# Performance work log

Measured on AMD Instinct MI355X. Metric: run time of the kernel, lower is better.

## Reference

```python
import jax, jax.numpy as jnp
import numpy as np

H_LAT = 64   # latent height (original_shape H)
W_LAT = 64   # latent width  (original_shape W)
COND_LEN = 77  # text tokens per regional condition


def _resize_nearest_exact(m, H, W):
    # matches torch F.interpolate(mode='nearest-exact') for a 2D mask
    h0, w0 = m.shape
    ih = jnp.floor((jnp.arange(H) + 0.5) * (h0 / H)).astype(jnp.int32)
    iw = jnp.floor((jnp.arange(W) + 0.5) * (w0 / W)).astype(jnp.int32)
    return m[ih][:, iw]


def setup_inputs() -> dict:
    key = jax.random.key(0)
    kq, kk, kv, km = jax.random.split(key, 4)
    b, qlen, inner = 2, H_LAT * W_LAT, 512
    klen = 4 * COND_LEN  # 4 regions x 77 tokens
    q = jax.random.normal(kq, (b, qlen, inner), dtype=jnp.float32)
    k = jax.random.normal(kk, (b, klen, inner), dtype=jnp.float32)
    v = jax.random.normal(kv, (b, klen, inner), dtype=jnp.float32)
    dd_masks = jax.random.uniform(km, (4, 32, 32), dtype=jnp.float32)
    # ensure full spatial coverage (region 0 = global) so no softmax row is all-masked
    dd_masks = dd_masks.at[0].set(1.0)
    return {"q": q, "k": k, "v": v, "dd_masks": dd_masks, "heads": 8}


def reference(q, k, v, dd_masks, heads):
    b, qlen, inner = q.shape
    dh = inner // heads
    # [b, heads, seq, dh]
    qh = q.reshape(b, qlen, heads, dh).transpose(0, 2, 1, 3)
    kh = k.reshape(b, -1, heads, dh).transpose(0, 2, 1, 3)
    vh = v.reshape(b, -1, heads, dh).transpose(0, 2, 1, 3)

    # build DenseDiffusion mask: each region mask resized to HxW, flattened,
    # and repeated over that region's COND_LEN key columns
    R = dd_masks.shape[0]
    resized = jax.vmap(lambda m: _resize_nearest_exact(m, H_LAT, W_LAT))(dd_masks)  # [R,H,W]
    flat = resized.reshape(R, H_LAT * W_LAT).T            # [HW, R]
    masks = jnp.repeat(flat, COND_LEN, axis=1)            # [HW, R*COND_LEN]
    mask_bool = masks > 0.5                               # [HW, klen]
    mask_scale = (H_LAT * W_LAT) / jnp.sum(masks, axis=0, keepdims=True)  # [1, klen]

    scale = 1.0 / np.sqrt(dh).astype(np.float32)
    attn = jnp.einsum('bhqd,bhkd->bhqk', qh, kh) * scale  # [b,h,HW,klen]
    attn = attn * mask_scale                              # broadcast over b,h,q
    attn = jnp.where(mask_bool, attn, -jnp.inf)
    w = jax.nn.softmax(attn, axis=-1)
    out = jnp.einsum('bhqk,bhkd->bhqd', w, vh)
    return out.transpose(0, 2, 1, 3).reshape(b, qlen, heads * dh)
```

## Files before the change

kernel.cpp:

```cpp
#include <hip/hip_runtime.h>
#include <hip/hip_bf16.h>

typedef __attribute__((ext_vector_type(8))) short short8;
typedef __attribute__((ext_vector_type(16))) float floatx16;

#define HW_TOK 4096
#define KLEN 308
#define DH 64
#define INNER 512

#define KROWS 320
#define VSTRU 328
#define VBASE (KROWS * 64)
#define KV_TOTAL (VBASE + DH * VSTRU)
#define NW 8

__device__ __forceinline__ unsigned short f2bf(float f) {
    union { float f; unsigned u; } x; x.f = f;
    unsigned u = x.u;
    return (unsigned short)((u + 0x7FFFu + ((u >> 16) & 1u)) >> 16);
}
__device__ __forceinline__ unsigned pk2bf(float a, float b) {
    return ((unsigned)f2bf(b) << 16) | (unsigned)f2bf(a);
}

__global__ __launch_bounds__(512, 1)
void dd_attn_kernel(const float* __restrict__ q,
                    const float* __restrict__ k,
                    const float* __restrict__ v,
                    const float* __restrict__ dd,
                    float* __restrict__ out) {
    __shared__ unsigned short KV[KV_TOTAL];
    __shared__ unsigned short Pb[NW][2][32][32];

    const int tid  = threadIdx.x;
    const int lane = tid & 63;
    const int wave = tid >> 6;
    const int half = lane >> 5;
    const int l31  = lane & 31;
    const int quad = lane >> 4;
    const int l15  = lane & 15;
    const int prot = 8 * ((l31 >> 1) & 7);

    const int bid = blockIdx.x;
    const int bh  = bid >> 4;
    const int grp = bid & 15;
    const int b = bh >> 3, h = bh & 7;

    const float* qp = q + (size_t)b * HW_TOK * INNER + h * DH;
    const float* kp = k + (size_t)b * KLEN * INNER + h * DH;
    const float* vp = v + (size_t)b * KLEN * INNER + h * DH;
    float* op = out + (size_t)b * HW_TOK * INNER + h * DH;

    for (int e = tid; e < KLEN * 32; e += 512) {
        int row = e >> 5, d2 = e & 31;
        float2 f = *(const float2*)(kp + (size_t)row * INNER + 2 * d2);
        int c = d2 >> 2;
        int off = row * 64 + (((c ^ (row & 7)) << 3) | ((d2 & 3) << 1));
        *(unsigned*)&KV[off] = pk2bf(f.x, f.y);
    }
    for (int e = tid; e < 12 * 64; e += 512) KV[KLEN * 64 + e] = 0;

    #pragma unroll
    for (int i = 0; i < 5; ++i) {
        int cq = wave + NW * i;
        float f[8];
        #pragma unroll
        for (int j = 0; j < 8; ++j) {
            int col = cq * 8 + j;
            f[j] = (col < KLEN) ? vp[(size_t)col * INNER + lane] : 0.f;
        }
        union { short8 s; unsigned u[4]; } vv;
        #pragma unroll
        for (int j = 0; j < 4; ++j) vv.u[j] = pk2bf(f[2 * j], f[2 * j + 1]);
        int swz = (cq & ~7) | ((cq ^ (lane & 7)) & 7);
        *(short8*)&KV[VBASE + lane * VSTRU + (swz << 3)] = vv.s;
    }
    float rsum = 0.f;
    {
        const float* dp = dd + quad * 1024 + l15 * 4;
        #pragma unroll
        for (int j = 0; j < 16; ++j) {
            float4 f = *(const float4*)(dp + j * 64);
            rsum += f.x + f.y + f.z + f.w;
        }
        #pragma unroll
        for (int off = 1; off < 16; off <<= 1) rsum += __shfl_xor(rsum, off);
    }
    float rsc[4];
    #pragma unroll
    for (int r = 0; r < 4; ++r)
        rsc[r] = 4096.0f / (4.0f * __shfl(rsum, r * 16 + l15));

    __syncthreads();

    const int q0 = (grp * NW + wave) * 32;
    const int qrow = q0 + l31;

    short8 qb[4];
    const float* qr = qp + (size_t)qrow * INNER;
    #pragma unroll
    for (int ks = 0; ks < 4; ++ks) {
        const float* p0 = qr + ks * 16 + half * 8;
        float4 a = *(const float4*)p0;
        float4 c = *(const float4*)(p0 + 4);
        union { short8 s; unsigned u[4]; } u;
        u.u[0] = pk2bf(a.x, a.y); u.u[1] = pk2bf(a.z, a.w);
        u.u[2] = pk2bf(c.x, c.y); u.u[3] = pk2bf(c.z, c.w);
        qb[ks] = u.s;
    }

    const int mi = (qrow >> 7) * 32 + ((qrow & 63) >> 1);
    float coef[4];
    #pragma unroll
    for (int r = 0; r < 4; ++r)
        coef[r] = (dd[r * 1024 + mi] > 0.5f) ? 0.125f * 1.44269504089f * rsc[r] : -1.0f;

    float l_run = 0.f;
    floatx16 oA[2], oB[2];
    #pragma unroll
    for (int j = 0; j < 16; ++j) { oA[0][j]=0.f; oA[1][j]=0.f; oB[0][j]=0.f; oB[1][j]=0.f; }

    #pragma unroll
    for (int t = 0; t < 10; ++t) {
        const int row = t * 32 + l31;
        floatx16 c;
        #pragma unroll
        for (int j = 0; j < 16; ++j) c[j] = 0.f;
        #pragma unroll
        for (int ks = 0; ks < 4; ++ks) {
            int cc = ks * 2 + half;
            short8 ka = *(const short8*)&KV[row * 64 + ((cc ^ (row & 7)) << 3)];
            c = __builtin_amdgcn_mfma_f32_32x32x16_bf16(ka, qb[ks], c, 0, 0, 0);
        }
        #pragma unroll
        for (int reg = 0; reg < 16; ++reg) {
            const int C0 = t * 32 + (reg & 3) + 8 * (reg >> 2);
            const int C1 = C0 + 4;
            float cfA = (C0 < 77) ? coef[0] : (C0 < 154) ? coef[1]
                      : (C0 < 231) ? coef[2] : (C0 < 308) ? coef[3] : -1.0f;
            float cfB = (C1 < 77) ? coef[0] : (C1 < 154) ? coef[1]
                      : (C1 < 231) ? coef[2] : (C1 < 308) ? coef[3] : -1.0f;
            float cf = half ? cfB : cfA;
            float p = __builtin_amdgcn_exp2f(c[reg] * cf);
            p = (cf > 0.f) ? p : 0.f;
            c[reg] = p;
            l_run += p;
        }
        const int tb = t & 1;
        unsigned short* pr = &Pb[wave][tb][l31][0];
        #pragma unroll
        for (int g = 0; g < 4; ++g) {
            unsigned u0 = pk2bf(c[4 * g],     c[4 * g + 1]);
            unsigned u1 = pk2bf(c[4 * g + 2], c[4 * g + 3]);
            *(uint2*)&pr[(8 * g + 4 * half + prot) & 31] = make_uint2(u0, u1);
        }
        #pragma unroll
        for (int ks2 = 0; ks2 < 2; ++ks2) {
            short8 pb = *(const short8*)&pr[(16 * ks2 + 8 * half + prot) & 31];
            int cc2 = (t * 2 + ks2) * 2 + half;
            #pragma unroll
            for (int mt = 0; mt < 2; ++mt) {
                int vrow = 32 * mt + l31;
                int swz = (cc2 & ~7) | ((cc2 ^ (vrow & 7)) & 7);
                short8 va = *(const short8*)&KV[VBASE + vrow * VSTRU + (swz << 3)];
                if (ks2 == 0)
                    oA[mt] = __builtin_amdgcn_mfma_f32_32x32x16_bf16(va, pb, oA[mt], 0, 0, 0);
                else
                    oB[mt] = __builtin_amdgcn_mfma_f32_32x32x16_bf16(va, pb, oB[mt], 0, 0, 0);
            }
        }
    }

    l_run += __shfl_xor(l_run, 32);
    const float inv = 1.0f / l_run;
    float* o = op + (size_t)qrow * INNER;
    #pragma unroll
    for (int mt = 0; mt < 2; ++mt) {
        #pragma unroll
        for (int g = 0; g < 4; ++g) {
            float4 ov;
            ov.x = (oA[mt][4 * g]     + oB[mt][4 * g])     * inv;
            ov.y = (oA[mt][4 * g + 1] + oB[mt][4 * g + 1]) * inv;
            ov.z = (oA[mt][4 * g + 2] + oB[mt][4 * g + 2]) * inv;
            ov.w = (oA[mt][4 * g + 3] + oB[mt][4 * g + 3]) * inv;
            *(float4*)&o[32 * mt + 8 * g + 4 * half] = ov;
        }
    }
}

extern "C" void kernel_launch(void* const* d_in, const int* in_sizes, int n_in,
                              void* d_out, int out_size, void* d_ws, size_t ws_size,
                              hipStream_t stream) {
    const float* q  = (const float*)d_in[0];
    const float* k  = (const float*)d_in[1];
    const float* v  = (const float*)d_in[2];
    const float* dd = (const float*)d_in[3];
    float* out = (float*)d_out;
    dd_attn_kernel<<<dim3(256), dim3(512), 0, stream>>>(q, k, v, dd, out);
}
```

Before: 103.9 us.

## Pass softmax probabilities via cross-lane shuffles instead of an LDS round trip

Drops the per-wave LDS buffer that held the bf16 probability tile. The P operand for the PV matmul is now built in registers with a 32-lane xor shuffle, and the MFMA operand order is swapped so the output accumulates transposed. That removes LDS writes and reads and one sync point per tile, and frees enough LDS for launch_bounds(512,2). The cost is more shuffle instructions, a tighter VGPR cap that may cause spills, and scalar coalesced output stores with a per-row shuffled normaliser. It also drops the K padding rows; their scores are masked to zero by the select.

Result: faster. 91.06 us (-12.3%).

```diff
diff --git a/kernel.cpp b/kernel.cpp
--- a/kernel.cpp
+++ b/kernel.cpp
@@ -9,9 +9,8 @@
 #define DH 64
 #define INNER 512
 
-#define KROWS 320
 #define VSTRU 328
-#define VBASE (KROWS * 64)
+#define VBASE (KLEN * 64)
 #define KV_TOTAL (VBASE + DH * VSTRU)
 #define NW 8
 
@@ -24,14 +23,13 @@
     return ((unsigned)f2bf(b) << 16) | (unsigned)f2bf(a);
 }
 
-__global__ __launch_bounds__(512, 1)
+__global__ __launch_bounds__(512, 2)
 void dd_attn_kernel(const float* __restrict__ q,
                     const float* __restrict__ k,
                     const float* __restrict__ v,
                     const float* __restrict__ dd,
                     float* __restrict__ out) {
     __shared__ unsigned short KV[KV_TOTAL];
-    __shared__ unsigned short Pb[NW][2][32][32];
 
     const int tid  = threadIdx.x;
     const int lane = tid & 63;
@@ -40,7 +38,6 @@
     const int l31  = lane & 31;
     const int quad = lane >> 4;
     const int l15  = lane & 15;
-    const int prot = 8 * ((l31 >> 1) & 7);
 
     const int bid = blockIdx.x;
     const int bh  = bid >> 4;
@@ -59,8 +56,6 @@
         int off = row * 64 + (((c ^ (row & 7)) << 3) | ((d2 & 3) << 1));
         *(unsigned*)&KV[off] = pk2bf(f.x, f.y);
     }
-    for (int e = tid; e < 12 * 64; e += 512) KV[KLEN * 64 + e] = 0;
-
     #pragma unroll
     for (int i = 0; i < 5; ++i) {
         int cq = wave + NW * i;
@@ -116,10 +111,10 @@
     for (int r = 0; r < 4; ++r)
         coef[r] = (dd[r * 1024 + mi] > 0.5f) ? 0.125f * 1.44269504089f * rsc[r] : -1.0f;
 
-    float l_run = 0.f;
-    floatx16 oA[2], oB[2];
+    float l0 = 0.f, l1 = 0.f, l2 = 0.f, l3 = 0.f;
+    floatx16 oacc[2];
     #pragma unroll
-    for (int j = 0; j < 16; ++j) { oA[0][j]=0.f; oA[1][j]=0.f; oB[0][j]=0.f; oB[1][j]=0.f; }
+    for (int j = 0; j < 16; ++j) { oacc[0][j] = 0.f; oacc[1][j] = 0.f; }
 
     #pragma unroll
     for (int t = 0; t < 10; ++t) {
@@ -145,47 +140,48 @@
             float p = __builtin_amdgcn_exp2f(c[reg] * cf);
             p = (cf > 0.f) ? p : 0.f;
             c[reg] = p;
-            l_run += p;
+            if ((reg & 3) == 0) l0 += p; else if ((reg & 3) == 1) l1 += p;
+            else if ((reg & 3) == 2) l2 += p; else l3 += p;
         }
-        const int tb = t & 1;
-        unsigned short* pr = &Pb[wave][tb][l31][0];
+        unsigned d[8], pd[8];
         #pragma unroll
-        for (int g = 0; g < 4; ++g) {
-            unsigned u0 = pk2bf(c[4 * g],     c[4 * g + 1]);
-            unsigned u1 = pk2bf(c[4 * g + 2], c[4 * g + 3]);
-            *(uint2*)&pr[(8 * g + 4 * half + prot) & 31] = make_uint2(u0, u1);
-        }
+        for (int g = 0; g < 8; ++g) d[g] = pk2bf(c[2 * g], c[2 * g + 1]);
+        #pragma unroll
+        for (int g = 0; g < 8; ++g) pd[g] = (unsigned)__shfl_xor((int)d[g], 32);
+        union { short8 s; unsigned u[4]; } f0, f1;
+        f0.u[0] = half ? pd[2] : d[0];
+        f0.u[1] = half ? pd[3] : d[1];
+        f0.u[2] = half ? d[2]  : pd[0];
+        f0.u[3] = half ? d[3]  : pd[1];
+        f1.u[0] = half ? pd[6] : d[4];
+        f1.u[1] = half ? pd[7] : d[5];
+        f1.u[2] = half ? d[6]  : pd[4];
+        f1.u[3] = half ? d[7]  : pd[5];
         #pragma unroll
         for (int ks2 = 0; ks2 < 2; ++ks2) {
-            short8 pb = *(const short8*)&pr[(16 * ks2 + 8 * half + prot) & 31];
+            short8 pa = ks2 ? f1.s : f0.s;
             int cc2 = (t * 2 + ks2) * 2 + half;
             #pragma unroll
             for (int mt = 0; mt < 2; ++mt) {
                 int vrow = 32 * mt + l31;
                 int swz = (cc2 & ~7) | ((cc2 ^ (vrow & 7)) & 7);
-                short8 va = *(const short8*)&KV[VBASE + vrow * VSTRU + (swz << 3)];
-                if (ks2 == 0)
-                    oA[mt] = __builtin_amdgcn_mfma_f32_32x32x16_bf16(va, pb, oA[mt], 0, 0, 0);
-                else
-                    oB[mt] = __builtin_amdgcn_mfma_f32_32x32x16_bf16(va, pb, oB[mt], 0, 0, 0);
+                short8 vb = *(const short8*)&KV[VBASE + vrow * VSTRU + (swz << 3)];
+                oacc[mt] = __builtin_amdgcn_mfma_f32_32x32x16_bf16(pa, vb, oacc[mt], 0, 0, 0);
             }
         }
     }
 
+    float l_run = (l0 + l1) + (l2 + l3);
     l_run += __shfl_xor(l_run, 32);
-    const float inv = 1.0f / l_run;
-    float* o = op + (size_t)qrow * INNER;
+
     #pragma unroll
-    for (int mt = 0; mt < 2; ++mt) {
-        #pragma unroll
-        for (int g = 0; g < 4; ++g) {
-            float4 ov;
-            ov.x = (oA[mt][4 * g]     + oB[mt][4 * g])     * inv;
-            ov.y = (oA[mt][4 * g + 1] + oB[mt][4 * g + 1]) * inv;
-            ov.z = (oA[mt][4 * g + 2] + oB[mt][4 * g + 2]) * inv;
-            ov.w = (oA[mt][4 * g + 3] + oB[mt][4 * g + 3]) * inv;
-            *(float4*)&o[32 * mt + 8 * g + 4 * half] = ov;
-        }
+    for (int reg = 0; reg < 16; ++reg) {
+        const int qrl = (reg & 3) + 8 * (reg >> 2) + 4 * half;
+        float lr = __shfl(l_run, qrl);
+        float inv = 1.0f / lr;
+        float* o = op + (size_t)(q0 + qrl) * INNER + l31;
+        o[0]  = oacc[0][reg] * inv;
+        o[32] = oacc[1][reg] * inv;
     }
 }
 
```
